# Optimization experiments

Measured on AMD Instinct MI355X. Metric: run time of the kernel, lower is better.

## Reference

```python
import jax, jax.numpy as jnp
import numpy as np

N_NODES = 50000

def spmm(rows, cols, vals, x):
    # sparse [n,n] @ dense [n,d] via gather + segment_sum
    gathered = vals[:, None] * x[cols]          # [E, d]
    return jax.ops.segment_sum(gathered, rows, num_segments=N_NODES)

def setup_inputs() -> dict:
    key = jax.random.key(0)
    k1, k2, k3, k4, k5, k6 = jax.random.split(key, 6)
    embeddings = jax.random.normal(k1, (N_NODES, 128), dtype=jnp.float32)
    adj_rows = jax.random.randint(k2, (800000,), 0, N_NODES, dtype=jnp.int32)
    adj_cols = jax.random.randint(k3, (800000,), 0, N_NODES, dtype=jnp.int32)
    adj_vals = jax.random.uniform(k4, (800000,), dtype=jnp.float32)
    W1 = jax.random.normal(k5, (128, 128), dtype=jnp.float32) * 0.05
    W2 = jax.random.normal(k6, (128, 64), dtype=jnp.float32) * 0.05
    return {"embeddings": embeddings, "adj_rows": adj_rows, "adj_cols": adj_cols,
            "adj_vals": adj_vals, "W1": W1, "W2": W2}

def reference(embeddings, adj_rows, adj_cols, adj_vals, W1, W2):
    # layer 1: SpMM -> dense GEMM -> ReLU
    h = jax.nn.relu(spmm(adj_rows, adj_cols, adj_vals, embeddings) @ W1)
    # layer 2: SpMM -> dense GEMM (no nonlinearity)
    logits = spmm(adj_rows, adj_cols, adj_vals, h) @ W2
    return jax.nn.softmax(logits, axis=1)
```

## Files before the change

kernel.cpp:

```cpp
#include <hip/hip_runtime.h>
#include <cmath>

#define N_NODES 50000
#define DIM 128
#define DOUT 64
#define SCAN_NB 196

typedef float f32x4 __attribute__((ext_vector_type(4)));

__device__ __forceinline__ unsigned short f2bf(float f) {
  unsigned int u = __float_as_uint(f);
  u = (u + 0x7fffu + ((u >> 16) & 1u)) >> 16;
  return (unsigned short)u;
}
__device__ __forceinline__ float bflo(unsigned int q) {
  return __uint_as_float(q << 16);
}
__device__ __forceinline__ float bfhi(unsigned int q) {
  return __uint_as_float(q & 0xffff0000u);
}


__global__ __launch_bounds__(256) void off_kernel(
    const int* __restrict__ rows, int* __restrict__ deg,
    int* __restrict__ localoff, int E) {
  int e = blockIdx.x * blockDim.x + threadIdx.x;
  if (e < E) localoff[e] = atomicAdd(&deg[rows[e]], 1);
}

__global__ __launch_bounds__(256) void scan_blk_kernel(
    const int* __restrict__ deg, int* __restrict__ incl,
    int* __restrict__ partials) {
  __shared__ int s[256];
  int i = blockIdx.x * 256 + threadIdx.x;
  int v = (i < N_NODES) ? deg[i] : 0;
  s[threadIdx.x] = v;
  __syncthreads();
  for (int o = 1; o < 256; o <<= 1) {
    int t = (threadIdx.x >= (unsigned)o) ? s[threadIdx.x - o] : 0;
    __syncthreads();
    s[threadIdx.x] += t;
    __syncthreads();
  }
  if (i < N_NODES) incl[i] = s[threadIdx.x];
  if (threadIdx.x == 255) partials[blockIdx.x] = s[255];
}

__global__ __launch_bounds__(256) void scan_part_kernel(
    int* __restrict__ partials, int* __restrict__ rowptr, int E) {
  __shared__ int s[256];
  int v = (threadIdx.x < SCAN_NB) ? partials[threadIdx.x] : 0;
  s[threadIdx.x] = v;
  __syncthreads();
  for (int o = 1; o < 256; o <<= 1) {
    int t = (threadIdx.x >= (unsigned)o) ? s[threadIdx.x - o] : 0;
    __syncthreads();
    s[threadIdx.x] += t;
    __syncthreads();
  }
  if (threadIdx.x < SCAN_NB) partials[threadIdx.x] = s[threadIdx.x] - v;
  if (threadIdx.x == 0) rowptr[N_NODES] = E;
}

__global__ __launch_bounds__(256) void scan_add_kernel(
    const int* __restrict__ incl, const int* __restrict__ deg,
    const int* __restrict__ partials, int* __restrict__ rowptr) {
  int i = blockIdx.x * 256 + threadIdx.x;
  if (i < N_NODES)
    rowptr[i] = incl[i] - deg[i] + partials[blockIdx.x];
}

__global__ __launch_bounds__(256) void scatter_kernel(
    const int* __restrict__ rows, const int* __restrict__ cols,
    const float* __restrict__ vals, const int* __restrict__ rowptr,
    const int* __restrict__ localoff, int2* __restrict__ edges, int E) {
  int e = blockIdx.x * blockDim.x + threadIdx.x;
  if (e < E) {
    int p = rowptr[rows[e]] + localoff[e];
    edges[p] = make_int2(cols[e], __float_as_int(vals[e]));
  }
}

template <int N, bool XBF16>
__global__ __launch_bounds__(256) void gemm_kernel(
    const void* __restrict__ xin, const float* __restrict__ W,
    unsigned short* __restrict__ y, int M) {
  __shared__ float sW[128 * 64];
  __shared__ float sX[64 * 132];
  const int cb = blockIdx.y;
  const int row0 = blockIdx.x * 64;

  for (int i = threadIdx.x; i < 128 * 16; i += 256) {
    int k = i >> 4, c4 = i & 15;
    reinterpret_cast<f32x4*>(sW)[k * 16 + c4] =
        reinterpret_cast<const f32x4*>(W)[k * (N / 4) + cb * 16 + c4];
  }
  if constexpr (XBF16) {
    const unsigned int* xq = (const unsigned int*)xin;
    for (int i = threadIdx.x; i < 64 * 16; i += 256) {
      int r = i >> 4, g = i & 15;
      int gr = row0 + r;
      if (gr >= M) gr = M - 1;
      uint4 q = reinterpret_cast<const uint4*>(xq + (size_t)gr * 64)[g];
      float* d = &sX[r * 132 + g * 8];
      d[0] = bflo(q.x); d[1] = bfhi(q.x);
      d[2] = bflo(q.y); d[3] = bfhi(q.y);
      d[4] = bflo(q.z); d[5] = bfhi(q.z);
      d[6] = bflo(q.w); d[7] = bfhi(q.w);
    }
  } else {
    const float* x = (const float*)xin;
    for (int i = threadIdx.x; i < 64 * 32; i += 256) {
      int r = i >> 5, c4 = i & 31;
      int gr = row0 + r;
      if (gr >= M) gr = M - 1;
      f32x4 v = reinterpret_cast<const f32x4*>(x + (size_t)gr * 128)[c4];
      *reinterpret_cast<f32x4*>(&sX[r * 132 + c4 * 4]) = v;
    }
  }
  __syncthreads();

  const int ct = threadIdx.x & 15;
  const int rt = threadIdx.x >> 4;
  const int c0 = ct * 4;
  float acc[4][4] = {};

  for (int k = 0; k < 128; k += 4) {
    f32x4 xa[4], wb[4];
#pragma unroll
    for (int r = 0; r < 4; ++r)
      xa[r] = *reinterpret_cast<const f32x4*>(&sX[(rt * 4 + r) * 132 + k]);
#pragma unroll
    for (int kk = 0; kk < 4; ++kk)
      wb[kk] = *reinterpret_cast<const f32x4*>(&sW[(k + kk) * 64 + c0]);
#pragma unroll
    for (int r = 0; r < 4; ++r)
#pragma unroll
      for (int c = 0; c < 4; ++c)
#pragma unroll
        for (int kk = 0; kk < 4; ++kk)
          acc[r][c] += xa[r][kk] * wb[kk][c];
  }

#pragma unroll
  for (int r = 0; r < 4; ++r) {
    int gr = row0 + rt * 4 + r;
    if (gr < M) {
      ushort4 v = {f2bf(acc[r][0]), f2bf(acc[r][1]),
                   f2bf(acc[r][2]), f2bf(acc[r][3])};
      *reinterpret_cast<ushort4*>(y + (size_t)gr * N + cb * 64 + c0) = v;
    }
  }
}

__global__ __launch_bounds__(256) void spmm_relu_kernel(
    const int* __restrict__ rowptr, const int2* __restrict__ edges,
    const unsigned int* __restrict__ t1q,
    unsigned int* __restrict__ hq) {
  const int row = blockIdx.x * 4 + (threadIdx.x >> 6);
  const int lane = threadIdx.x & 63;
  const int beg = rowptr[row];
  const int end = rowptr[row + 1];
  float ax = 0.f, ay = 0.f;
  int i = beg;
  for (; i + 8 <= end; i += 8) {
    int2 e0 = edges[i],     e1 = edges[i + 1], e2 = edges[i + 2], e3 = edges[i + 3];
    int2 e4 = edges[i + 4], e5 = edges[i + 5], e6 = edges[i + 6], e7 = edges[i + 7];
    unsigned int q0 = t1q[(size_t)e0.x * 64 + lane];
    unsigned int q1 = t1q[(size_t)e1.x * 64 + lane];
    unsigned int q2 = t1q[(size_t)e2.x * 64 + lane];
    unsigned int q3 = t1q[(size_t)e3.x * 64 + lane];
    unsigned int q4 = t1q[(size_t)e4.x * 64 + lane];
    unsigned int q5 = t1q[(size_t)e5.x * 64 + lane];
    unsigned int q6 = t1q[(size_t)e6.x * 64 + lane];
    unsigned int q7 = t1q[(size_t)e7.x * 64 + lane];
    float w0 = __int_as_float(e0.y), w1 = __int_as_float(e1.y);
    float w2 = __int_as_float(e2.y), w3 = __int_as_float(e3.y);
    float w4 = __int_as_float(e4.y), w5 = __int_as_float(e5.y);
    float w6 = __int_as_float(e6.y), w7 = __int_as_float(e7.y);
    ax += w0 * bflo(q0) + w1 * bflo(q1) + w2 * bflo(q2) + w3 * bflo(q3) +
          w4 * bflo(q4) + w5 * bflo(q5) + w6 * bflo(q6) + w7 * bflo(q7);
    ay += w0 * bfhi(q0) + w1 * bfhi(q1) + w2 * bfhi(q2) + w3 * bfhi(q3) +
          w4 * bfhi(q4) + w5 * bfhi(q5) + w6 * bfhi(q6) + w7 * bfhi(q7);
  }
  for (; i + 2 <= end; i += 2) {
    int2 e0 = edges[i], e1 = edges[i + 1];
    unsigned int q0 = t1q[(size_t)e0.x * 64 + lane];
    unsigned int q1 = t1q[(size_t)e1.x * 64 + lane];
    float w0 = __int_as_float(e0.y), w1 = __int_as_float(e1.y);
    ax += w0 * bflo(q0) + w1 * bflo(q1);
    ay += w0 * bfhi(q0) + w1 * bfhi(q1);
  }
  if (i < end) {
    int2 e = edges[i];
    unsigned int q = t1q[(size_t)e.x * 64 + lane];
    float w = __int_as_float(e.y);
    ax += w * bflo(q);
    ay += w * bfhi(q);
  }
  ax = fmaxf(ax, 0.f);
  ay = fmaxf(ay, 0.f);
  hq[(size_t)row * 64 + lane] =
      (unsigned int)f2bf(ax) | ((unsigned int)f2bf(ay) << 16);
}

__global__ __launch_bounds__(256) void spmm_softmax_kernel(
    const int* __restrict__ rowptr, const int2* __restrict__ edges,
    const unsigned int* __restrict__ t2q,
    float* __restrict__ out) {
  const int row = blockIdx.x * 4 + (threadIdx.x >> 6);
  const int lane = threadIdx.x & 63;
  const int sub = lane >> 5;
  const int sl = lane & 31;
  const int beg = rowptr[row];
  const int end = rowptr[row + 1];
  float ax = 0.f, ay = 0.f;
  int i = beg;
  for (; i + 8 <= end; i += 8) {
    int2 ea = edges[i + sub];
    int2 eb = edges[i + 2 + sub];
    int2 ec = edges[i + 4 + sub];
    int2 ed = edges[i + 6 + sub];
    unsigned int qa = t2q[(size_t)ea.x * 32 + sl];
    unsigned int qb = t2q[(size_t)eb.x * 32 + sl];
    unsigned int qc = t2q[(size_t)ec.x * 32 + sl];
    unsigned int qd = t2q[(size_t)ed.x * 32 + sl];
    float va = __int_as_float(ea.y), vb = __int_as_float(eb.y);
    float vc = __int_as_float(ec.y), vd = __int_as_float(ed.y);
    ax += va * bflo(qa) + vb * bflo(qb) + vc * bflo(qc) + vd * bflo(qd);
    ay += va * bfhi(qa) + vb * bfhi(qb) + vc * bfhi(qc) + vd * bfhi(qd);
  }
  for (; i < end; i += 2) {
    int j = i + sub;
    bool ok = j < end;
    int2 e = edges[ok ? j : end - 1];
    float v = ok ? __int_as_float(e.y) : 0.f;
    unsigned int q = t2q[(size_t)e.x * 32 + sl];
    ax += v * bflo(q);
    ay += v * bfhi(q);
  }
  ax += __shfl_xor(ax, 32);
  ay += __shfl_xor(ay, 32);
  float m = fmaxf(ax, ay);
  for (int o = 16; o >= 1; o >>= 1) m = fmaxf(m, __shfl_xor(m, o));
  float ex = expf(ax - m), ey = expf(ay - m);
  float s = ex + ey;
  for (int o = 16; o >= 1; o >>= 1) s += __shfl_xor(s, o);
  if (sub == 0)
    reinterpret_cast<float2*>(out)[(size_t)row * 32 + sl] =
        make_float2(ex / s, ey / s);
}

extern "C" void kernel_launch(void* const* d_in, const int* in_sizes, int n_in,
                              void* d_out, int out_size, void* d_ws, size_t ws_size,
                              hipStream_t stream) {
  const float* emb   = (const float*)d_in[0];
  const int*   arows = (const int*)d_in[1];
  const int*   acols = (const int*)d_in[2];
  const float* avals = (const float*)d_in[3];
  const float* W1    = (const float*)d_in[4];
  const float* W2    = (const float*)d_in[5];
  float* out = (float*)d_out;
  const int E = in_sizes[1];

  const size_t hbytes = (size_t)N_NODES * DIM * sizeof(float);
  char* p = (char*)d_ws;
  char*  bufA   = p;         p += hbytes;
  char*  bufB   = p;         p += hbytes;
  int2*  edges  = (int2*)p;  p += (size_t)E * sizeof(int2);
  int*   deg    = (int*)p;   p += (size_t)N_NODES * sizeof(int);
  int*   rowptr = (int*)p;
  int* incl     = (int*)edges;
  int* partials = ((int*)edges) + N_NODES;
  int* localoff = (int*)bufB;

  hipMemsetAsync(deg, 0, (size_t)N_NODES * sizeof(int), stream);

  const int eblocks = (E + 255) / 256;

  off_kernel<<<eblocks, 256, 0, stream>>>(arows, deg, localoff, E);
  scan_blk_kernel<<<SCAN_NB, 256, 0, stream>>>(deg, incl, partials);
  scan_part_kernel<<<1, 256, 0, stream>>>(partials, rowptr, E);
  scan_add_kernel<<<SCAN_NB, 256, 0, stream>>>(incl, deg, partials, rowptr);
  scatter_kernel<<<eblocks, 256, 0, stream>>>(arows, acols, avals, rowptr,
                                              localoff, edges, E);

  const int gblocks = (N_NODES + 63) / 64;

  gemm_kernel<128, false><<<dim3(gblocks, 2), 256, 0, stream>>>(
      emb, W1, (unsigned short*)bufA, N_NODES);
  spmm_relu_kernel<<<N_NODES / 4, 256, 0, stream>>>(
      rowptr, edges, (const unsigned int*)bufA, (unsigned int*)bufB);
  gemm_kernel<64, true><<<dim3(gblocks, 1), 256, 0, stream>>>(
      bufB, W2, (unsigned short*)bufA, N_NODES);
  spmm_softmax_kernel<<<N_NODES / 4, 256, 0, stream>>>(
      rowptr, edges, (const unsigned int*)bufA, out);
}
```

Measured before the change: 248.9 us.

## Replace FP32 SIMT GEMMs with split-bf16 MFMA GEMMs and pre-transposed weights

Replaces the scalar FP32 shared-memory GEMMs with bf16 MFMA 16x16x32 matrix-core GEMMs. To keep accuracy close to FP32, both weights and the FP32 input are split into high and low bf16 parts and combined with two or three MFMAs per tile. A small new kernel transposes and splits W1/W2 into bf16 hi/lo once per call. This trades extra MFMA work and a launch for much higher matrix throughput. The output store becomes scattered 2-byte writes, which may cost bandwidth.

```diff
diff --git a/kernel.cpp b/kernel.cpp
--- a/kernel.cpp
+++ b/kernel.cpp
@@ -7,11 +7,16 @@
 #define SCAN_NB 196
 
 typedef float f32x4 __attribute__((ext_vector_type(4)));
+typedef short bf16x8 __attribute__((ext_vector_type(8)));
+typedef float f32x4v __attribute__((ext_vector_type(4)));
 
 __device__ __forceinline__ unsigned short f2bf(float f) {
   unsigned int u = __float_as_uint(f);
   u = (u + 0x7fffu + ((u >> 16) & 1u)) >> 16;
   return (unsigned short)u;
+}
+__device__ __forceinline__ float bf2f(unsigned short h) {
+  return __uint_as_float((unsigned int)h << 16);
 }
 __device__ __forceinline__ float bflo(unsigned int q) {
   return __uint_as_float(q << 16);
@@ -81,74 +86,113 @@
   }
 }
 
-template <int N, bool XBF16>
-__global__ __launch_bounds__(256) void gemm_kernel(
-    const void* __restrict__ xin, const float* __restrict__ W,
-    unsigned short* __restrict__ y, int M) {
-  __shared__ float sW[128 * 64];
-  __shared__ float sX[64 * 132];
+__global__ __launch_bounds__(256) void wtrans_kernel(
+    const float* __restrict__ W1, const float* __restrict__ W2,
+    unsigned short* __restrict__ W1th, unsigned short* __restrict__ W1tl,
+    unsigned short* __restrict__ W2th, unsigned short* __restrict__ W2tl) {
+  int i = blockIdx.x * 256 + threadIdx.x;
+  if (i < 128 * 128) {
+    int c = i >> 7, k = i & 127;
+    float v = W1[k * 128 + c];
+    unsigned short h = f2bf(v);
+    W1th[i] = h;
+    W1tl[i] = f2bf(v - bf2f(h));
+  } else if (i < 128 * 128 + 64 * 128) {
+    int j = i - 128 * 128;
+    int c = j >> 7, k = j & 127;
+    float v = W2[k * 64 + c];
+    unsigned short h = f2bf(v);
+    W2th[j] = h;
+    W2tl[j] = f2bf(v - bf2f(h));
+  }
+}
+
+template <int N, bool XSPLIT>
+__global__ __launch_bounds__(256) void gemm_mfma_kernel(
+    const void* __restrict__ xin,
+    const unsigned short* __restrict__ Wth,
+    const unsigned short* __restrict__ Wtl,
+    unsigned short* __restrict__ y,
+    int M) {
+  __shared__ unsigned short sXh[64 * 136];
+  __shared__ unsigned short sXl[XSPLIT ? 64 * 136 : 1];
+  __shared__ unsigned short sWh[64 * 136];
+  __shared__ unsigned short sWl[64 * 136];
   const int cb = blockIdx.y;
   const int row0 = blockIdx.x * 64;
-
-  for (int i = threadIdx.x; i < 128 * 16; i += 256) {
-    int k = i >> 4, c4 = i & 15;
-    reinterpret_cast<f32x4*>(sW)[k * 16 + c4] =
-        reinterpret_cast<const f32x4*>(W)[k * (N / 4) + cb * 16 + c4];
-  }
-  if constexpr (XBF16) {
-    const unsigned int* xq = (const unsigned int*)xin;
-    for (int i = threadIdx.x; i < 64 * 16; i += 256) {
+  const int tid = threadIdx.x;
+
+  if constexpr (XSPLIT) {
+    const float* x = (const float*)xin;
+    for (int i = tid; i < 64 * 16; i += 256) {
       int r = i >> 4, g = i & 15;
-      int gr = row0 + r;
-      if (gr >= M) gr = M - 1;
-      uint4 q = reinterpret_cast<const uint4*>(xq + (size_t)gr * 64)[g];
-      float* d = &sX[r * 132 + g * 8];
-      d[0] = bflo(q.x); d[1] = bfhi(q.x);
-      d[2] = bflo(q.y); d[3] = bfhi(q.y);
-      d[4] = bflo(q.z); d[5] = bfhi(q.z);
-      d[6] = bflo(q.w); d[7] = bfhi(q.w);
+      int gr = row0 + r; if (gr >= M) gr = M - 1;
+      const f32x4* src = reinterpret_cast<const f32x4*>(x + (size_t)gr * 128 + g * 8);
+      f32x4 a = src[0], b = src[1];
+      unsigned short* dh = &sXh[r * 136 + g * 8];
+      unsigned short* dl = &sXl[r * 136 + g * 8];
+      float v[8] = {a.x, a.y, a.z, a.w, b.x, b.y, b.z, b.w};
+#pragma unroll
+      for (int j = 0; j < 8; ++j) {
+        unsigned short h = f2bf(v[j]);
+        dh[j] = h;
+        dl[j] = f2bf(v[j] - bf2f(h));
+      }
     }
   } else {
-    const float* x = (const float*)xin;
-    for (int i = threadIdx.x; i < 64 * 32; i += 256) {
-      int r = i >> 5, c4 = i & 31;
-      int gr = row0 + r;
-      if (gr >= M) gr = M - 1;
-      f32x4 v = reinterpret_cast<const f32x4*>(x + (size_t)gr * 128)[c4];
-      *reinterpret_cast<f32x4*>(&sX[r * 132 + c4 * 4]) = v;
+    const uint4* xq = (const uint4*)xin;
+    for (int i = tid; i < 64 * 16; i += 256) {
+      int r = i >> 4, g = i & 15;
+      int gr = row0 + r; if (gr >= M) gr = M - 1;
+      *reinterpret_cast<uint4*>(&sXh[r * 136 + g * 8]) = xq[(size_t)gr * 16 + g];
+    }
+  }
+  {
+    const uint4* wh = (const uint4*)Wth;
+    const uint4* wl = (const uint4*)Wtl;
+    for (int i = tid; i < 64 * 16; i += 256) {
+      int c = i >> 4, g = i & 15;
+      size_t src = (size_t)(cb * 64 + c) * 16 + g;
+      *reinterpret_cast<uint4*>(&sWh[c * 136 + g * 8]) = wh[src];
+      *reinterpret_cast<uint4*>(&sWl[c * 136 + g * 8]) = wl[src];
     }
   }
   __syncthreads();
 
-  const int ct = threadIdx.x & 15;
-  const int rt = threadIdx.x >> 4;
-  const int c0 = ct * 4;
-  float acc[4][4] = {};
-
-  for (int k = 0; k < 128; k += 4) {
-    f32x4 xa[4], wb[4];
-#pragma unroll
-    for (int r = 0; r < 4; ++r)
-      xa[r] = *reinterpret_cast<const f32x4*>(&sX[(rt * 4 + r) * 132 + k]);
-#pragma unroll
-    for (int kk = 0; kk < 4; ++kk)
-      wb[kk] = *reinterpret_cast<const f32x4*>(&sW[(k + kk) * 64 + c0]);
-#pragma unroll
-    for (int r = 0; r < 4; ++r)
-#pragma unroll
-      for (int c = 0; c < 4; ++c)
-#pragma unroll
-        for (int kk = 0; kk < 4; ++kk)
-          acc[r][c] += xa[r][kk] * wb[kk][c];
-  }
-
-#pragma unroll
-  for (int r = 0; r < 4; ++r) {
-    int gr = row0 + rt * 4 + r;
-    if (gr < M) {
-      ushort4 v = {f2bf(acc[r][0]), f2bf(acc[r][1]),
-                   f2bf(acc[r][2]), f2bf(acc[r][3])};
-      *reinterpret_cast<ushort4*>(y + (size_t)gr * N + cb * 64 + c0) = v;
+  const int lane = tid & 63;
+  const int w = tid >> 6;
+  const int r = lane & 15;
+  const int q = lane >> 4;
+
+  bf16x8 ah[4], al[4];
+#pragma unroll
+  for (int k = 0; k < 4; ++k) {
+    ah[k] = *reinterpret_cast<const bf16x8*>(&sXh[(w * 16 + r) * 136 + k * 32 + q * 8]);
+    if constexpr (XSPLIT)
+      al[k] = *reinterpret_cast<const bf16x8*>(&sXl[(w * 16 + r) * 136 + k * 32 + q * 8]);
+  }
+
+  f32x4v acc[4] = {{0.f,0.f,0.f,0.f},{0.f,0.f,0.f,0.f},{0.f,0.f,0.f,0.f},{0.f,0.f,0.f,0.f}};
+#pragma unroll
+  for (int k = 0; k < 4; ++k) {
+#pragma unroll
+    for (int n = 0; n < 4; ++n) {
+      bf16x8 bh = *reinterpret_cast<const bf16x8*>(&sWh[(n * 16 + r) * 136 + k * 32 + q * 8]);
+      bf16x8 bl = *reinterpret_cast<const bf16x8*>(&sWl[(n * 16 + r) * 136 + k * 32 + q * 8]);
+      acc[n] = __builtin_amdgcn_mfma_f32_16x16x32_bf16(ah[k], bh, acc[n], 0, 0, 0);
+      acc[n] = __builtin_amdgcn_mfma_f32_16x16x32_bf16(ah[k], bl, acc[n], 0, 0, 0);
+      if constexpr (XSPLIT)
+        acc[n] = __builtin_amdgcn_mfma_f32_16x16x32_bf16(al[k], bh, acc[n], 0, 0, 0);
+    }
+  }
+
+#pragma unroll
+  for (int n = 0; n < 4; ++n) {
+#pragma unroll
+    for (int j = 0; j < 4; ++j) {
+      int gr = row0 + w * 16 + q * 4 + j;
+      if (gr < M)
+        y[(size_t)gr * N + cb * 64 + n * 16 + r] = f2bf(acc[n][j]);
     }
   }
 }
@@ -269,7 +313,11 @@
   char*  bufB   = p;         p += hbytes;
   int2*  edges  = (int2*)p;  p += (size_t)E * sizeof(int2);
   int*   deg    = (int*)p;   p += (size_t)N_NODES * sizeof(int);
-  int*   rowptr = (int*)p;
+  int*   rowptr = (int*)p;   p += (size_t)(N_NODES + 1) * sizeof(int);
+  unsigned short* W1th = (unsigned short*)p; p += 128 * 128 * 2;
+  unsigned short* W1tl = (unsigned short*)p; p += 128 * 128 * 2;
+  unsigned short* W2th = (unsigned short*)p; p += 64 * 128 * 2;
+  unsigned short* W2tl = (unsigned short*)p; p += 64 * 128 * 2;
   int* incl     = (int*)edges;
   int* partials = ((int*)edges) + N_NODES;
   int* localoff = (int*)bufB;
@@ -277,6 +325,8 @@
   hipMemsetAsync(deg, 0, (size_t)N_NODES * sizeof(int), stream);
 
   const int eblocks = (E + 255) / 256;
+
+  wtrans_kernel<<<96, 256, 0, stream>>>(W1, W2, W1th, W1tl, W2th, W2tl);
 
   off_kernel<<<eblocks, 256, 0, stream>>>(arows, deg, localoff, E);
   scan_blk_kernel<<<SCAN_NB, 256, 0, stream>>>(deg, incl, partials);
@@ -287,12 +337,12 @@
 
   const int gblocks = (N_NODES + 63) / 64;
 
-  gemm_kernel<128, false><<<dim3(gblocks, 2), 256, 0, stream>>>(
-      emb, W1, (unsigned short*)bufA, N_NODES);
+  gemm_mfma_kernel<128, true><<<dim3(gblocks, 2), 256, 0, stream>>>(
+      emb, W1th, W1tl, (unsigned short*)bufA, N_NODES);
   spmm_relu_kernel<<<N_NODES / 4, 256, 0, stream>>>(
       rowptr, edges, (const unsigned int*)bufA, (unsigned int*)bufB);
-  gemm_kernel<64, true><<<dim3(gblocks, 1), 256, 0, stream>>>(
-      bufB, W2, (unsigned short*)bufA, N_NODES);
+  gemm_mfma_kernel<64, false><<<dim3(gblocks, 1), 256, 0, stream>>>(
+      bufB, W2th, W2tl, (unsigned short*)bufA, N_NODES);
   spmm_softmax_kernel<<<N_NODES / 4, 256, 0, stream>>>(
       rowptr, edges, (const unsigned int*)bufA, out);
 }
```

After: 232.7 us. 6.5% less time.
